# Kernel optimization log

Hardware: AMD Instinct MI355X
Metric: run time of the kernel (lower is better)

The kernel has to match this reference:

```python
import jax, jax.numpy as jnp
import numpy as np

B, N, D = 16, 2048, 64

def setup_inputs() -> dict:
    key = jax.random.key(0)
    kq, kk, kv = jax.random.split(key, 3)
    queries = jax.random.normal(kq, (B, N, D), dtype=jnp.float32)
    keys = jax.random.normal(kk, (B, N, D), dtype=jnp.float32)
    values = jax.random.normal(kv, (B, N, D), dtype=jnp.float32)
    scaling_factor = jnp.asarray(np.sqrt(D), dtype=jnp.float32)
    return {"queries": queries, "keys": keys, "values": values, "scaling_factor": scaling_factor}

def reference(queries, keys, values, scaling_factor):
    # scores: [B, N, N] = Q K^T / scale
    scores = jnp.einsum('bqd,bkd->bqk', queries, keys) / scaling_factor
    atn = jax.nn.softmax(scores, axis=2)
    return jnp.einsum('bqk,bkd->bqd', atn, values)
```

## Files before the change

kernel.cpp:

```cpp
#include <hip/hip_runtime.h>
#include <hip/hip_bf16.h>

#define BATCH 16
#define SEQ 2048
#define DIM 64

typedef __attribute__((ext_vector_type(8))) __bf16 bf16x8;
typedef __attribute__((ext_vector_type(8))) unsigned short u16x8;
typedef __attribute__((ext_vector_type(2))) unsigned int u32x2;
typedef __attribute__((ext_vector_type(4))) unsigned int u32x4;
typedef __attribute__((ext_vector_type(16))) float f32x16;

#if __has_builtin(__builtin_amdgcn_exp2f)
#define EXP2F(x) __builtin_amdgcn_exp2f(x)
#else
#define EXP2F(x) __expf(0.69314718055994531f * (x))
#endif

__device__ __forceinline__ unsigned short f2bf_hw(float f) {
    __bf16 h = (__bf16)f;
    return __builtin_bit_cast(unsigned short, h);
}

__device__ __forceinline__ unsigned int pk_bf16(float lo, float hi) {
    unsigned int a = f2bf_hw(lo), b = f2bf_hw(hi);
    return a | (b << 16);
}

__device__ __forceinline__ bf16x8 ld_bf8_g(const unsigned short* p) {
    u16x8 u = *(const u16x8*)p;
    return __builtin_bit_cast(bf16x8, u);
}

__device__ __forceinline__ void half_swap(unsigned int a, unsigned int b,
                                          unsigned int& lo, unsigned int& hi) {
#if __has_builtin(__builtin_amdgcn_permlane32_swap)
    u32x2 r = __builtin_amdgcn_permlane32_swap(a, b, false, false);
    lo = r[0];
    hi = r[1];
#else
    unsigned int sa = (unsigned int)__shfl_xor((int)a, 32);
    unsigned int sb = (unsigned int)__shfl_xor((int)b, 32);
    const bool hh = (threadIdx.x & 32) != 0;
    lo = hh ? sb : a;
    hi = hh ? b : sa;
#endif
}

__global__ __launch_bounds__(256)
void preconvert_kv(const float* __restrict__ K, const float* __restrict__ V,
                   unsigned short* __restrict__ Ks, unsigned short* __restrict__ Vts) {
    __shared__ float vt[128 * 65];
    const int tid = threadIdx.x;
    if (blockIdx.x < 256) {
        const int b = blockIdx.x >> 4;
        const int t = blockIdx.x & 15;
        const float* src = K + ((size_t)(b * SEQ + t * 128)) * DIM;
        unsigned short* dst = Ks + ((size_t)(b * 16 + t)) * 8192;
        #pragma unroll
        for (int p = 0; p < 4; ++p) {
            const int cid = p * 256 + tid;
            const int key = cid >> 3, g = cid & 7;
            const int d0 = (g >> 1) * 16 + (g & 1) * 8;
            float4 x0 = *(const float4*)(src + key * DIM + d0);
            float4 x1 = *(const float4*)(src + key * DIM + d0 + 4);
            u16x8 o;
            o[0] = f2bf_hw(x0.x); o[1] = f2bf_hw(x0.y); o[2] = f2bf_hw(x0.z); o[3] = f2bf_hw(x0.w);
            o[4] = f2bf_hw(x1.x); o[5] = f2bf_hw(x1.y); o[6] = f2bf_hw(x1.z); o[7] = f2bf_hw(x1.w);
            *(u16x8*)(dst + (g * 128 + key) * 8) = o;
        }
    } else {
        const int vb = blockIdx.x - 256;
        const int b = vb >> 4;
        const int t = vb & 15;
        const float* src = V + ((size_t)(b * SEQ + t * 128)) * DIM;
        #pragma unroll
        for (int p = 0; p < 8; ++p) {
            const int f = p * 256 + tid;
            const int row = f >> 4, c4 = (f & 15) << 2;
            float4 x = *(const float4*)(src + row * DIM + c4);
            vt[row * 65 + c4 + 0] = x.x; vt[row * 65 + c4 + 1] = x.y;
            vt[row * 65 + c4 + 2] = x.z; vt[row * 65 + c4 + 3] = x.w;
        }
        __syncthreads();
        unsigned short* dst = Vts + ((size_t)(b * 16 + t)) * 8192;
        #pragma unroll
        for (int p = 0; p < 4; ++p) {
            const int cid = p * 256 + tid;
            const int g = cid >> 6, d = cid & 63;
            const int k0 = (g >> 1) * 16 + (g & 1) * 8;
            u16x8 o;
            #pragma unroll
            for (int j = 0; j < 8; ++j) o[j] = f2bf_hw(vt[(k0 + j) * 65 + d]);
            *(u16x8*)(dst + (g * 64 + d) * 8) = o;
        }
    }
}

__global__ __launch_bounds__(256, 3)
void attn_flash_kernel(const float* __restrict__ Q,
                       const unsigned short* __restrict__ Ks,
                       const unsigned short* __restrict__ Vts,
                       const float* __restrict__ scaling,
                       float* __restrict__ O) {
    __shared__ float comb[3 * 64 * 33];

    const int tid  = threadIdx.x;
    const int w    = tid >> 6;
    const int lane = tid & 63;
    const int m    = lane & 31;
    const int h    = lane >> 5;

    const int x  = blockIdx.x;
    const int b  = ((x & 7) << 1) | ((x >> 3) & 1);
    const int q0 = (x >> 4) * 32;

    const float csc = 1.4426950408889634f / scaling[0];

    bf16x8 aq[4];
    {
        const float* qsrc = Q + ((size_t)(b * SEQ + q0 + m)) * DIM + h * 8;
        #pragma unroll
        for (int c = 0; c < 4; ++c) {
            float4 x0 = *(const float4*)(qsrc + c * 16);
            float4 x1 = *(const float4*)(qsrc + c * 16 + 4);
            u32x4 pk;
            pk[0] = pk_bf16(x0.x * csc, x0.y * csc);
            pk[1] = pk_bf16(x0.z * csc, x0.w * csc);
            pk[2] = pk_bf16(x1.x * csc, x1.y * csc);
            pk[3] = pk_bf16(x1.z * csc, x1.w * csc);
            aq[c] = __builtin_bit_cast(bf16x8, pk);
        }
    }

    f32x16 Oacc[2];
    #pragma unroll
    for (int dt = 0; dt < 2; ++dt)
        #pragma unroll
        for (int r = 0; r < 16; ++r) Oacc[dt][r] = 0.f;
    float psum = 0.f;

    const unsigned short* Kbase = Ks + ((size_t)(b * 16 + w * 4)) * 8192;
    const unsigned short* Vbase = Vts + ((size_t)(b * 16 + w * 4)) * 8192;

    bf16x8 kcA[4], kcB[4];
    bf16x8 bv[2][2];
    f32x16 S;
    bf16x8 pb[2];

    auto load_k = [&](bf16x8* dst, int s) {
        const unsigned short* Kt = Kbase + (size_t)(s >> 2) * 8192;
        const int t = s & 3;
        #pragma unroll
        for (int c = 0; c < 4; ++c)
            dst[c] = ld_bf8_g(&Kt[((c * 2 + h) * 128 + t * 32 + m) * 8]);
    };
    auto load_v = [&](int s) {
        const unsigned short* Vt = Vbase + (size_t)(s >> 2) * 8192;
        const int t = s & 3;
        #pragma unroll
        for (int c2 = 0; c2 < 2; ++c2)
            #pragma unroll
            for (int dt = 0; dt < 2; ++dt)
                bv[c2][dt] = ld_bf8_g(&Vt[(((2 * t + c2) * 2 + h) * 64 + dt * 32 + m) * 8]);
    };
    auto calc_s = [&](const bf16x8* kc) {
        #pragma unroll
        for (int r = 0; r < 16; ++r) S[r] = 0.f;
        #pragma unroll
        for (int c = 0; c < 4; ++c)
            S = __builtin_amdgcn_mfma_f32_32x32x16_bf16(kc[c], aq[c], S, 0, 0, 0);
    };
    auto exp_swap = [&]() {
        unsigned int d0[8];
        #pragma unroll
        for (int k = 0; k < 4; ++k) {
            float a0 = EXP2F(S[4 * k + 0]), a1 = EXP2F(S[4 * k + 1]);
            float a2 = EXP2F(S[4 * k + 2]), a3 = EXP2F(S[4 * k + 3]);
            psum += (a0 + a1) + (a2 + a3);
            d0[2 * k + 0] = pk_bf16(a0, a1);
            d0[2 * k + 1] = pk_bf16(a2, a3);
        }
        #pragma unroll
        for (int c2 = 0; c2 < 2; ++c2) {
            u32x4 bw;
            unsigned int lo, hi;
            half_swap(d0[4 * c2 + 0], d0[4 * c2 + 2], lo, hi);
            bw[0] = lo; bw[2] = hi;
            half_swap(d0[4 * c2 + 1], d0[4 * c2 + 3], lo, hi);
            bw[1] = lo; bw[3] = hi;
            pb[c2] = __builtin_bit_cast(bf16x8, bw);
        }
    };
    auto pv = [&]() {
        __builtin_amdgcn_s_setprio(1);
        #pragma unroll
        for (int c2 = 0; c2 < 2; ++c2)
            #pragma unroll
            for (int dt = 0; dt < 2; ++dt)
                Oacc[dt] = __builtin_amdgcn_mfma_f32_32x32x16_bf16(bv[c2][dt], pb[c2], Oacc[dt], 0, 0, 0);
        __builtin_amdgcn_s_setprio(0);
    };

    load_k(kcA, 0);
    load_k(kcB, 1);
    load_v(0);
    calc_s(kcA);

    #pragma unroll 1
    for (int it = 0; it < 8; ++it) {
        const int e = 2 * it;
        {
            const int s2 = (e + 2 < 16) ? e + 2 : 15;
            load_k(kcA, s2);
            exp_swap();
            calc_s(kcB);
            pv();
            load_v(e + 1);
        }
        {
            const int s3 = (e + 3 < 16) ? e + 3 : 15;
            load_k(kcB, s3);
            exp_swap();
            calc_s(kcA);
            pv();
            const int s2 = (e + 2 < 16) ? e + 2 : 15;
            load_v(s2);
        }
    }

    float l = psum + __shfl_xor(psum, 32);
    if (w > 0) {
        float* dst = comb + ((w - 1) * 64 + lane) * 33;
        #pragma unroll
        for (int dt = 0; dt < 2; ++dt)
            #pragma unroll
            for (int r = 0; r < 16; ++r)
                dst[dt * 16 + r] = Oacc[dt][r];
        dst[32] = l;
    }
    __syncthreads();
    if (w == 0) {
        const float* p0 = comb + (0 * 64 + lane) * 33;
        const float* p1 = comb + (1 * 64 + lane) * 33;
        const float* p2 = comb + (2 * 64 + lane) * 33;
        const float invl = 1.0f / (l + p0[32] + p1[32] + p2[32]);
        float* orow = O + ((size_t)(b * SEQ + q0 + m)) * DIM;
        #pragma unroll
        for (int dt = 0; dt < 2; ++dt) {
            #pragma unroll
            for (int k = 0; k < 4; ++k) {
                float4 o4;
                #pragma unroll
                for (int j = 0; j < 4; ++j) {
                    const int r = 4 * k + j;
                    ((float*)&o4)[j] = (Oacc[dt][r] + p0[dt * 16 + r] + p1[dt * 16 + r]
                                        + p2[dt * 16 + r]) * invl;
                }
                *(float4*)(orow + dt * 32 + 8 * k + 4 * h) = o4;
            }
        }
    }
}

extern "C" void kernel_launch(void* const* d_in, const int* in_sizes, int n_in,
                              void* d_out, int out_size, void* d_ws, size_t ws_size,
                              hipStream_t stream) {
    const float* Q = (const float*)d_in[0];
    const float* K = (const float*)d_in[1];
    const float* V = (const float*)d_in[2];
    const float* scaling = (const float*)d_in[3];
    float* O = (float*)d_out;

    unsigned short* Ks  = (unsigned short*)d_ws;
    unsigned short* Vts = Ks + (size_t)BATCH * 16 * 8192;

    preconvert_kv<<<dim3(512), dim3(256), 0, stream>>>(K, V, Ks, Vts);
    attn_flash_kernel<<<dim3(BATCH * (SEQ / 32)), dim3(256), 0, stream>>>(Q, Ks, Vts, scaling, O);
}
```

Before: 103.0 us.

## Share K/V tiles across 4 query warps via LDS ring buffer, 128 queries per block

Each block now handles 128 queries, one 32-row query tile per warp, instead of 32 queries split across warps by key range. K/V tiles are loaded cooperatively from global memory into a 3-slot LDS ring with register prefetch, and each tile is shared by all four warps. This cuts global K/V traffic by about 4x and removes the cross-warp combine step. The cost is a block-wide barrier every step, only 256 blocks (one wave on the device, so less latency hiding), and dropped occupancy hints; the preconvert block order is also interleaved by batch.

```diff
diff --git a/kernel.cpp b/kernel.cpp
--- a/kernel.cpp
+++ b/kernel.cpp
@@ -25,11 +25,6 @@
 __device__ __forceinline__ unsigned int pk_bf16(float lo, float hi) {
     unsigned int a = f2bf_hw(lo), b = f2bf_hw(hi);
     return a | (b << 16);
-}
-
-__device__ __forceinline__ bf16x8 ld_bf8_g(const unsigned short* p) {
-    u16x8 u = *(const u16x8*)p;
-    return __builtin_bit_cast(bf16x8, u);
 }
 
 __device__ __forceinline__ void half_swap(unsigned int a, unsigned int b,
@@ -52,9 +47,11 @@
                    unsigned short* __restrict__ Ks, unsigned short* __restrict__ Vts) {
     __shared__ float vt[128 * 65];
     const int tid = threadIdx.x;
-    if (blockIdx.x < 256) {
-        const int b = blockIdx.x >> 4;
-        const int t = blockIdx.x & 15;
+    const int x = blockIdx.x;
+    const int b = ((x & 7) << 1) | ((x >> 3) & 1);
+    const int kpath = (x >> 4) & 1;
+    const int t = x >> 5;
+    if (kpath) {
         const float* src = K + ((size_t)(b * SEQ + t * 128)) * DIM;
         unsigned short* dst = Ks + ((size_t)(b * 16 + t)) * 8192;
         #pragma unroll
@@ -70,17 +67,14 @@
             *(u16x8*)(dst + (g * 128 + key) * 8) = o;
         }
     } else {
-        const int vb = blockIdx.x - 256;
-        const int b = vb >> 4;
-        const int t = vb & 15;
         const float* src = V + ((size_t)(b * SEQ + t * 128)) * DIM;
         #pragma unroll
         for (int p = 0; p < 8; ++p) {
             const int f = p * 256 + tid;
             const int row = f >> 4, c4 = (f & 15) << 2;
-            float4 x = *(const float4*)(src + row * DIM + c4);
-            vt[row * 65 + c4 + 0] = x.x; vt[row * 65 + c4 + 1] = x.y;
-            vt[row * 65 + c4 + 2] = x.z; vt[row * 65 + c4 + 3] = x.w;
+            float4 xv = *(const float4*)(src + row * DIM + c4);
+            vt[row * 65 + c4 + 0] = xv.x; vt[row * 65 + c4 + 1] = xv.y;
+            vt[row * 65 + c4 + 2] = xv.z; vt[row * 65 + c4 + 3] = xv.w;
         }
         __syncthreads();
         unsigned short* dst = Vts + ((size_t)(b * 16 + t)) * 8192;
@@ -97,13 +91,13 @@
     }
 }
 
-__global__ __launch_bounds__(256, 3)
+__global__ __launch_bounds__(256)
 void attn_flash_kernel(const float* __restrict__ Q,
                        const unsigned short* __restrict__ Ks,
                        const unsigned short* __restrict__ Vts,
                        const float* __restrict__ scaling,
                        float* __restrict__ O) {
-    __shared__ float comb[3 * 64 * 33];
+    __shared__ __attribute__((aligned(16))) unsigned short ring[3 * 4096];
 
     const int tid  = threadIdx.x;
     const int w    = tid >> 6;
@@ -113,13 +107,13 @@
 
     const int x  = blockIdx.x;
     const int b  = ((x & 7) << 1) | ((x >> 3) & 1);
-    const int q0 = (x >> 4) * 32;
+    const int q0 = (x >> 4) * 128;
 
     const float csc = 1.4426950408889634f / scaling[0];
 
     bf16x8 aq[4];
     {
-        const float* qsrc = Q + ((size_t)(b * SEQ + q0 + m)) * DIM + h * 8;
+        const float* qsrc = Q + ((size_t)(b * SEQ + q0 + w * 32 + m)) * DIM + h * 8;
         #pragma unroll
         for (int c = 0; c < 4; ++c) {
             float4 x0 = *(const float4*)(qsrc + c * 16);
@@ -140,38 +134,48 @@
         for (int r = 0; r < 16; ++r) Oacc[dt][r] = 0.f;
     float psum = 0.f;
 
-    const unsigned short* Kbase = Ks + ((size_t)(b * 16 + w * 4)) * 8192;
-    const unsigned short* Vbase = Vts + ((size_t)(b * 16 + w * 4)) * 8192;
-
-    bf16x8 kcA[4], kcB[4];
-    bf16x8 bv[2][2];
-    f32x16 S;
-    bf16x8 pb[2];
-
-    auto load_k = [&](bf16x8* dst, int s) {
-        const unsigned short* Kt = Kbase + (size_t)(s >> 2) * 8192;
-        const int t = s & 3;
+    const unsigned short* Kb = Ks  + ((size_t)b * 16) * 8192;
+    const unsigned short* Vb = Vts + ((size_t)b * 16) * 8192;
+    const int qq = 2 * w + h;
+
+    auto ld_k_g = [&](int s) -> u16x8 {
+        const int it = s >> 2, tt = s & 3;
+        return *(const u16x8*)(Kb + (size_t)it * 8192 +
+                               (size_t)((qq * 128 + tt * 32 + m)) * 8);
+    };
+    auto ld_v_g = [&](int s) -> u16x8 {
+        const int it = s >> 2, tt = s & 3;
+        return *(const u16x8*)(Vb + (size_t)it * 8192 +
+                               (size_t)((((2 * tt + (qq >> 2)) * 2 + ((qq >> 1) & 1)) * 64 +
+                                         (qq & 1) * 32 + m)) * 8);
+    };
+    auto st_lds = [&](int slot, u16x8 kv, u16x8 vv) {
+        *(u16x8*)(&ring[slot * 4096 + w * 512 + lane * 8]) = kv;
+        *(u16x8*)(&ring[slot * 4096 + 2048 + w * 512 + lane * 8]) = vv;
+    };
+    auto ld_kc = [&](int slot, bf16x8* kc) {
         #pragma unroll
         for (int c = 0; c < 4; ++c)
-            dst[c] = ld_bf8_g(&Kt[((c * 2 + h) * 128 + t * 32 + m) * 8]);
-    };
-    auto load_v = [&](int s) {
-        const unsigned short* Vt = Vbase + (size_t)(s >> 2) * 8192;
-        const int t = s & 3;
+            kc[c] = __builtin_bit_cast(bf16x8,
+                *(const u16x8*)(&ring[slot * 4096 + (c * 2 + h) * 256 + m * 8]));
+    };
+    auto ld_bv = [&](int slot, bf16x8 (*bv)[2]) {
         #pragma unroll
         for (int c2 = 0; c2 < 2; ++c2)
             #pragma unroll
             for (int dt = 0; dt < 2; ++dt)
-                bv[c2][dt] = ld_bf8_g(&Vt[(((2 * t + c2) * 2 + h) * 64 + dt * 32 + m) * 8]);
-    };
-    auto calc_s = [&](const bf16x8* kc) {
+                bv[c2][dt] = __builtin_bit_cast(bf16x8,
+                    *(const u16x8*)(&ring[slot * 4096 + 2048 +
+                                          (c2 * 4 + h * 2 + dt) * 256 + m * 8]));
+    };
+    auto calc_s = [&](const bf16x8* kc, f32x16& S) {
         #pragma unroll
         for (int r = 0; r < 16; ++r) S[r] = 0.f;
         #pragma unroll
         for (int c = 0; c < 4; ++c)
             S = __builtin_amdgcn_mfma_f32_32x32x16_bf16(kc[c], aq[c], S, 0, 0, 0);
     };
-    auto exp_swap = [&]() {
+    auto exp_swap = [&](const f32x16& S, bf16x8* pbo) {
         unsigned int d0[8];
         #pragma unroll
         for (int k = 0; k < 4; ++k) {
@@ -189,76 +193,87 @@
             bw[0] = lo; bw[2] = hi;
             half_swap(d0[4 * c2 + 1], d0[4 * c2 + 3], lo, hi);
             bw[1] = lo; bw[3] = hi;
-            pb[c2] = __builtin_bit_cast(bf16x8, bw);
-        }
-    };
-    auto pv = [&]() {
-        __builtin_amdgcn_s_setprio(1);
+            pbo[c2] = __builtin_bit_cast(bf16x8, bw);
+        }
+    };
+    auto pv = [&](bf16x8 (*bv)[2], bf16x8* pb) {
         #pragma unroll
         for (int c2 = 0; c2 < 2; ++c2)
             #pragma unroll
             for (int dt = 0; dt < 2; ++dt)
                 Oacc[dt] = __builtin_amdgcn_mfma_f32_32x32x16_bf16(bv[c2][dt], pb[c2], Oacc[dt], 0, 0, 0);
-        __builtin_amdgcn_s_setprio(0);
-    };
-
-    load_k(kcA, 0);
-    load_k(kcB, 1);
-    load_v(0);
-    calc_s(kcA);
-
+    };
+
+    u16x8 rgK = ld_k_g(0), rgV = ld_v_g(0);
+    u16x8 nK  = ld_k_g(1), nV  = ld_v_g(1);
+    st_lds(0, rgK, rgV);
+    rgK = nK; rgV = nV;
+    asm volatile("s_waitcnt lgkmcnt(0)" ::: "memory");
+    __builtin_amdgcn_sched_barrier(0);
+    __builtin_amdgcn_s_barrier();
+    __builtin_amdgcn_sched_barrier(0);
+
+    bf16x8 bvH[2][2];
+    bf16x8 pbH[2];
+    {
+        const u32x4 z = {0u, 0u, 0u, 0u};
+        #pragma unroll
+        for (int c2 = 0; c2 < 2; ++c2) {
+            pbH[c2] = __builtin_bit_cast(bf16x8, z);
+            #pragma unroll
+            for (int dt = 0; dt < 2; ++dt) bvH[c2][dt] = __builtin_bit_cast(bf16x8, z);
+        }
+    }
+
+    int sl = 0;
     #pragma unroll 1
-    for (int it = 0; it < 8; ++it) {
-        const int e = 2 * it;
-        {
-            const int s2 = (e + 2 < 16) ? e + 2 : 15;
-            load_k(kcA, s2);
-            exp_swap();
-            calc_s(kcB);
-            pv();
-            load_v(e + 1);
-        }
-        {
-            const int s3 = (e + 3 < 16) ? e + 3 : 15;
-            load_k(kcB, s3);
-            exp_swap();
-            calc_s(kcA);
-            pv();
-            const int s2 = (e + 2 < 16) ? e + 2 : 15;
-            load_v(s2);
-        }
+    for (int t = 0; t < 63; ++t) {
+        const int s2 = (t + 2 < 64) ? t + 2 : 63;
+        u16x8 aK = ld_k_g(s2), aV = ld_v_g(s2);
+
+        pv(bvH, pbH);
+
+        bf16x8 kc[4];
+        ld_kc(sl, kc);
+        f32x16 S;
+        calc_s(kc, S);
+        ld_bv(sl, bvH);
+        exp_swap(S, pbH);
+
+        const int wslot = (sl == 2) ? 0 : sl + 1;
+        st_lds(wslot, rgK, rgV);
+        rgK = aK; rgV = aV;
+
+        asm volatile("s_waitcnt lgkmcnt(0)" ::: "memory");
+        __builtin_amdgcn_sched_barrier(0);
+        __builtin_amdgcn_s_barrier();
+        __builtin_amdgcn_sched_barrier(0);
+        sl = wslot;
+    }
+
+    {
+        pv(bvH, pbH);
+        bf16x8 kc[4];
+        ld_kc(sl, kc);
+        f32x16 S;
+        calc_s(kc, S);
+        ld_bv(sl, bvH);
+        exp_swap(S, pbH);
+        pv(bvH, pbH);
     }
 
     float l = psum + __shfl_xor(psum, 32);
-    if (w > 0) {
-        float* dst = comb + ((w - 1) * 64 + lane) * 33;
-        #pragma unroll
-        for (int dt = 0; dt < 2; ++dt)
-            #pragma unroll
-            for (int r = 0; r < 16; ++r)
-                dst[dt * 16 + r] = Oacc[dt][r];
-        dst[32] = l;
-    }
-    __syncthreads();
-    if (w == 0) {
-        const float* p0 = comb + (0 * 64 + lane) * 33;
-        const float* p1 = comb + (1 * 64 + lane) * 33;
-        const float* p2 = comb + (2 * 64 + lane) * 33;
-        const float invl = 1.0f / (l + p0[32] + p1[32] + p2[32]);
-        float* orow = O + ((size_t)(b * SEQ + q0 + m)) * DIM;
-        #pragma unroll
-        for (int dt = 0; dt < 2; ++dt) {
-            #pragma unroll
-            for (int k = 0; k < 4; ++k) {
-                float4 o4;
-                #pragma unroll
-                for (int j = 0; j < 4; ++j) {
-                    const int r = 4 * k + j;
-                    ((float*)&o4)[j] = (Oacc[dt][r] + p0[dt * 16 + r] + p1[dt * 16 + r]
-                                        + p2[dt * 16 + r]) * invl;
-                }
-                *(float4*)(orow + dt * 32 + 8 * k + 4 * h) = o4;
-            }
+    const float invl = 1.0f / l;
+    float* orow = O + ((size_t)(b * SEQ + q0 + w * 32 + m)) * DIM;
+    #pragma unroll
+    for (int dt = 0; dt < 2; ++dt) {
+        #pragma unroll
+        for (int k = 0; k < 4; ++k) {
+            float4 o4;
+            #pragma unroll
+            for (int j = 0; j < 4; ++j)
+                ((float*)&o4)[j] = Oacc[dt][4 * k + j] * invl;
+            *(float4*)(orow + dt * 32 + 8 * k + 4 * h) = o4;
         }
     }
 }
@@ -276,5 +291,5 @@
     unsigned short* Vts = Ks + (size_t)BATCH * 16 * 8192;
 
     preconvert_kv<<<dim3(512), dim3(256), 0, stream>>>(K, V, Ks, Vts);
-    attn_flash_kernel<<<dim3(BATCH * (SEQ / 32)), dim3(256), 0, stream>>>(Q, Ks, Vts, scaling, O);
-}
+    attn_flash_kernel<<<dim3(256), dim3(256), 0, stream>>>(Q, Ks, Vts, scaling, O);
+}
```

After: 112.5 us. +9.3%, slower.
